# Optimization experiments

Measured on AMD Instinct MI355X. Metric: run time of the kernel, lower is better.

Reference implementation:

```python
import jax, jax.numpy as jnp
import numpy as np

T, B, I, H, O, L = 256, 128, 128, 512, 1, 5


def setup_inputs() -> dict:
    key = jax.random.key(0)
    ks = jax.random.split(key, 12)
    k = 1.0 / np.sqrt(H)
    u = lambda kk, shape: jax.random.uniform(kk, shape, jnp.float32, -k, k)
    inp = {
        "input_seq": jax.random.normal(ks[0], (T, B, I), jnp.float32),
        # layer 0: input size I, 2 directions
        "W_ih0": u(ks[1], (2, 3 * H, I)),
        "W_hh0": u(ks[2], (2, 3 * H, H)),
        "b_ih0": u(ks[3], (2, 3 * H)),
        "b_hh0": u(ks[4], (2, 3 * H)),
        # layers 1..4: input size 2H, 2 directions
        "W_ih": u(ks[5], (L - 1, 2, 3 * H, 2 * H)),
        "W_hh": u(ks[6], (L - 1, 2, 3 * H, H)),
        "b_ih": u(ks[7], (L - 1, 2, 3 * H)),
        "b_hh": u(ks[8], (L - 1, 2, 3 * H)),
        "fc_w": u(ks[9], (O, 2 * H)),
        "fc_b": u(ks[10], (O,)),
    }
    return inp


def _gru_dir(x, Wih, Whh, bih, bhh):
    # x: [T, B, in]; precompute input-side gates for all timesteps
    gx = jnp.einsum('tbi,gi->tbg', x, Wih) + bih  # [T, B, 3H]

    def step(h, g):
        gh = h @ Whh.T + bhh  # [B, 3H]
        xr, xz, xn = jnp.split(g, 3, axis=-1)
        hr, hz, hn = jnp.split(gh, 3, axis=-1)
        r = jax.nn.sigmoid(xr + hr)
        z = jax.nn.sigmoid(xz + hz)
        n = jnp.tanh(xn + r * hn)
        h_new = (1.0 - z) * n + z * h
        return h_new, h_new

    h0 = jnp.zeros((x.shape[1], Whh.shape[1]), x.dtype)
    _, hs = jax.lax.scan(step, h0, gx)
    return hs  # [T, B, H]


def _bigru_layer(x, Wih, Whh, bih, bhh):
    # Wih: [2, 3H, in]; direction 0 = forward, 1 = backward (PyTorch convention)
    fwd = _gru_dir(x, Wih[0], Whh[0], bih[0], bhh[0])
    bwd = _gru_dir(x[::-1], Wih[1], Whh[1], bih[1], bhh[1])[::-1]
    return jnp.concatenate([fwd, bwd], axis=-1)  # [T, B, 2H]


def reference(input_seq, W_ih0, W_hh0, b_ih0, b_hh0, W_ih, W_hh, b_ih, b_hh, fc_w, fc_b):
    # 5-layer bidirectional GRU (eval mode: inter-layer dropout inactive)
    h = _bigru_layer(input_seq, W_ih0, W_hh0, b_ih0, b_hh0)
    for l in range(L - 1):
        h = _bigru_layer(h, W_ih[l], W_hh[l], b_ih[l], b_hh[l])
    out = jnp.einsum('tbh,oh->tbo', h, fc_w) + fc_b
    return jax.nn.sigmoid(out)
```

## Files before the change

kernel.cpp:

```cpp
#include <hip/hip_runtime.h>
#include <hip/hip_bf16.h>

#define T_ 256
#define B_ 128
#define H_ 512
#define G3 1536
#define SCH 32
#define NCH 8
#define RWG 32
#define BGRP 8

typedef __attribute__((ext_vector_type(8))) short short8;
typedef __attribute__((ext_vector_type(4))) short short4v;
typedef __attribute__((ext_vector_type(4))) float f32x4;

static __device__ __forceinline__ float b2f(short s){
    unsigned u = ((unsigned)(unsigned short)s) << 16;
    return __builtin_bit_cast(float, u);
}
static __device__ __forceinline__ short f2b(float f){
    __hip_bfloat16 h = __float2bfloat16(f);
    return __builtin_bit_cast(short, h);
}
static __device__ __forceinline__ void gload16(const void* g, void* l){
    __builtin_amdgcn_global_load_lds(
        (__attribute__((address_space(1))) void*)(void*)g,
        (__attribute__((address_space(3))) void*)l, 16, 0, 0);
}
static __device__ __forceinline__ short8 gload_sc(const short* p){
    short8 v;
    asm volatile("global_load_dwordx4 %0, %1, off sc0 sc1"
                 : "=v"(v) : "v"(p) : "memory");
    return v;
}
static __device__ __forceinline__ void gstore_sc(short* p, short v){
    asm volatile("global_store_short %0, %1, off sc0 sc1"
                 :: "v"(p), "v"(v) : "memory");
}
static __device__ __forceinline__ void wait_vm0(){
    asm volatile("s_waitcnt vmcnt(0)" ::: "memory");
}

__global__ void cvt_f32_to_bf16(const float* __restrict__ src, short* __restrict__ dst, int n){
    int i = (blockIdx.x * blockDim.x + threadIdx.x) * 4;
    int stride = gridDim.x * blockDim.x * 4;
    for (; i + 3 < n; i += stride){
        float4 v = *(const float4*)(src + i);
        short4v o;
        o[0] = f2b(v.x); o[1] = f2b(v.y); o[2] = f2b(v.z); o[3] = f2b(v.w);
        *(short4v*)(dst + i) = o;
    }
}

__global__ __launch_bounds__(256) void gx_gemm(
    const short* __restrict__ A,
    const short* __restrict__ W,
    const float* __restrict__ bias,
    short* __restrict__ gxc,
    int K, int t0f, int t0b_lo)
{
    __shared__ __align__(16) short sA[4096];
    __shared__ __align__(16) short sB[4096];
    const int dir = blockIdx.z;
    const int t0 = dir ? t0b_lo : t0f;
    const int m0 = blockIdx.x * 128;
    const int n0 = blockIdx.y * 128;
    const short* Ae = A + (size_t)(t0 * B_) * K;
    const short* We = W + (size_t)dir * G3 * K;
    short* out = gxc + (size_t)dir * ((size_t)SCH * B_ * G3);

    const int tid = threadIdx.x, wv = tid >> 6, lane = tid & 63;
    const int moff = (wv & 1) * 64, noff = (wv >> 1) * 64;
    const int e0 = wv * 1024 + lane * 8, e1 = e0 + 512;
    const short* a0 = Ae + (size_t)(m0 + (e0 >> 5)) * K + (e0 & 31);
    const short* a1 = Ae + (size_t)(m0 + (e1 >> 5)) * K + (e1 & 31);
    const short* b0 = We + (size_t)(n0 + (e0 >> 5)) * K + (e0 & 31);
    const short* b1 = We + (size_t)(n0 + (e1 >> 5)) * K + (e1 & 31);
    short* sa0 = &sA[wv * 1024];  short* sa1 = &sA[wv * 1024 + 512];
    short* sb0 = &sB[wv * 1024];  short* sb1 = &sB[wv * 1024 + 512];

    f32x4 acc[4][4] = {};
    const int lr = lane & 15, lk = (lane >> 4) * 8;

    for (int kk = 0; kk < K; kk += 32){
        gload16(a0 + kk, sa0); gload16(a1 + kk, sa1);
        gload16(b0 + kk, sb0); gload16(b1 + kk, sb1);
        __syncthreads();
        short8 ar[4], br[4];
        #pragma unroll
        for (int i = 0; i < 4; ++i) ar[i] = *(const short8*)&sA[(moff + i*16 + lr) * 32 + lk];
        #pragma unroll
        for (int i = 0; i < 4; ++i) br[i] = *(const short8*)&sB[(noff + i*16 + lr) * 32 + lk];
        #pragma unroll
        for (int ai = 0; ai < 4; ++ai)
            #pragma unroll
            for (int bi = 0; bi < 4; ++bi)
                acc[ai][bi] = __builtin_amdgcn_mfma_f32_16x16x32_bf16(ar[ai], br[bi], acc[ai][bi], 0, 0, 0);
        __syncthreads();
    }

    #pragma unroll
    for (int ai = 0; ai < 4; ++ai){
        #pragma unroll
        for (int bi = 0; bi < 4; ++bi){
            int col = n0 + noff + bi*16 + lr;
            float bv = bias[dir * G3 + col];
            #pragma unroll
            for (int r = 0; r < 4; ++r){
                int row = m0 + moff + ai*16 + ((lane >> 4) << 2) + r;
                out[(size_t)row * G3 + col] = f2b(acc[ai][bi][r] + bv);
            }
        }
    }
}

__global__ __launch_bounds__(256, 1) void rec_kernel(
    const short* __restrict__ gxc,
    const short* __restrict__ Whh,
    const float* __restrict__ bhh,
    short* __restrict__ xout,
    float* __restrict__ hfm,
    short* __restrict__ hbb,
    int* __restrict__ bar,
    int t0f, int t0b_hi, int first, int base)
{
    __shared__ __align__(16) short lds_h[32 * 520];
    const int tid = threadIdx.x, wv = tid >> 6, lane = tid & 63;
    const int ug = blockIdx.x >> 2, bg = blockIdx.x & 3, dir = blockIdx.y;
    const int u0 = ug * 64 + wv * 16;
    const int m0 = bg * 32;
    const int lr = lane & 15, lk = (lane >> 4) * 8;
    const int crow = (lane >> 4) * 4;

    const short* Wd = Whh + (size_t)dir * G3 * H_;
    short8 wreg[3][16];
    #pragma unroll
    for (int g = 0; g < 3; ++g)
        #pragma unroll
        for (int kk = 0; kk < 16; ++kk)
            wreg[g][kk] = *(const short8*)&Wd[(size_t)(g*H_ + u0 + lr) * H_ + kk*32 + lk];

    float bh[3];
    #pragma unroll
    for (int g = 0; g < 3; ++g) bh[g] = bhh[dir*G3 + g*H_ + u0 + lr];

    float hreg[2][4];
    #pragma unroll
    for (int mt = 0; mt < 2; ++mt)
        #pragma unroll
        for (int r = 0; r < 4; ++r)
            hreg[mt][r] = first ? 0.f
                : hfm[((size_t)dir*B_ + m0 + mt*16 + crow + r)*H_ + u0 + lr];

    int* cnt = bar + (dir*4 + bg) * 32;
    const short* gxd = gxc + (size_t)dir * ((size_t)SCH * B_ * G3);

    const int srow = tid >> 3, scol0 = (tid & 7) * 8;

    float gv[3][2][4];
    {
        const int tl0 = dir ? (SCH - 1) : 0;
        const short* gb = gxd + ((size_t)(tl0 * B_) + m0 + crow) * G3 + u0 + lr;
        #pragma unroll
        for (int g = 0; g < 3; ++g)
            #pragma unroll
            for (int mt = 0; mt < 2; ++mt)
                #pragma unroll
                for (int r = 0; r < 4; ++r)
                    gv[g][mt][r] = b2f(gb[(size_t)(mt*16 + r) * G3 + g * H_]);
    }

    for (int sl = 0; sl < SCH; ++sl){
        const int t  = dir ? (t0b_hi - sl) : (t0f + sl);
        const int rp = sl & 1;

        {
            const short* hsrc = hbb + ((size_t)(rp*2 + dir) * B_ + m0) * H_;
            short8 hv[8];
            #pragma unroll
            for (int c = 0; c < 8; ++c)
                hv[c] = gload_sc(hsrc + (size_t)srow * H_ + scol0 + c*64);
            wait_vm0();
            #pragma unroll
            for (int c = 0; c < 8; ++c)
                *(short8*)&lds_h[srow * 520 + scol0 + c*64] = hv[c];
        }
        __syncthreads();

        f32x4 acc[3][2] = {};
        #pragma unroll
        for (int kk = 0; kk < 16; ++kk){
            short8 a0 = *(const short8*)&lds_h[(lr)      * 520 + kk*32 + lk];
            short8 a1 = *(const short8*)&lds_h[(16 + lr) * 520 + kk*32 + lk];
            #pragma unroll
            for (int g = 0; g < 3; ++g){
                acc[g][0] = __builtin_amdgcn_mfma_f32_16x16x32_bf16(a0, wreg[g][kk], acc[g][0], 0, 0, 0);
                acc[g][1] = __builtin_amdgcn_mfma_f32_16x16x32_bf16(a1, wreg[g][kk], acc[g][1], 0, 0, 0);
            }
        }

        short* hwr = hbb + ((size_t)((rp^1)*2 + dir) * B_) * H_;
        #pragma unroll
        for (int mt = 0; mt < 2; ++mt){
            #pragma unroll
            for (int r = 0; r < 4; ++r){
                float gr = acc[0][mt][r] + bh[0] + gv[0][mt][r];
                float gz = acc[1][mt][r] + bh[1] + gv[1][mt][r];
                float gn = acc[2][mt][r] + bh[2];
                float xn = gv[2][mt][r];
                float rg = 1.f / (1.f + __expf(-gr));
                float zg = 1.f / (1.f + __expf(-gz));
                float e2 = __expf(2.f * (xn + rg * gn));
                float ng = 1.f - 2.f / (e2 + 1.f);
                float hn = (1.f - zg) * ng + zg * hreg[mt][r];
                hreg[mt][r] = hn;
                short h16 = f2b(hn);
                const int row = m0 + mt*16 + crow + r;
                gstore_sc(hwr + (size_t)row * H_ + u0 + lr, h16);
                xout[((size_t)t * B_ + row) * 1024 + dir*H_ + u0 + lr] = h16;
            }
        }

        wait_vm0();
        __syncthreads();
        if (tid == 0)
            __hip_atomic_fetch_add(cnt, 1, __ATOMIC_RELAXED, __HIP_MEMORY_SCOPE_AGENT);

        if (sl + 1 < SCH){
            const int tln = dir ? (SCH - 2 - sl) : (sl + 1);
            const short* gb = gxd + ((size_t)(tln * B_) + m0 + crow) * G3 + u0 + lr;
            #pragma unroll
            for (int g = 0; g < 3; ++g)
                #pragma unroll
                for (int mt = 0; mt < 2; ++mt)
                    #pragma unroll
                    for (int r = 0; r < 4; ++r)
                        gv[g][mt][r] = b2f(gb[(size_t)(mt*16 + r) * G3 + g * H_]);
        }

        if (tid == 0){
            const int tgt = (base + sl + 1) * BGRP;
            while (__hip_atomic_load(cnt, __ATOMIC_RELAXED, __HIP_MEMORY_SCOPE_AGENT) < tgt)
                __builtin_amdgcn_s_sleep(1);
        }
        __syncthreads();
    }

    #pragma unroll
    for (int mt = 0; mt < 2; ++mt)
        #pragma unroll
        for (int r = 0; r < 4; ++r)
            hfm[((size_t)dir*B_ + m0 + mt*16 + crow + r)*H_ + u0 + lr] = hreg[mt][r];
}

__global__ void fc_kernel(const short* __restrict__ h, const float* __restrict__ w,
                          const float* __restrict__ b, float* __restrict__ out){
    int wid = threadIdx.x >> 6, lane = threadIdx.x & 63;
    int tb = blockIdx.x * 4 + wid;
    const short* hp = h + (size_t)tb * 1024 + lane * 16;
    float s = 0.f;
    #pragma unroll
    for (int c = 0; c < 2; ++c){
        short8 v = *(const short8*)(hp + c * 8);
        #pragma unroll
        for (int e = 0; e < 8; ++e) s += b2f(v[e]) * w[lane * 16 + c * 8 + e];
    }
    #pragma unroll
    for (int o = 32; o; o >>= 1) s += __shfl_down(s, o);
    if (lane == 0) out[tb] = 1.f / (1.f + __expf(-(s + b[0])));
}

extern "C" void kernel_launch(void* const* d_in, const int* in_sizes, int n_in,
                              void* d_out, int out_size, void* d_ws, size_t ws_size,
                              hipStream_t stream){
    const float* input_seq = (const float*)d_in[0];
    const float* W_ih0 = (const float*)d_in[1];
    const float* W_hh0 = (const float*)d_in[2];
    const float* b_ih0 = (const float*)d_in[3];
    const float* b_hh0 = (const float*)d_in[4];
    const float* W_ih  = (const float*)d_in[5];
    const float* W_hh  = (const float*)d_in[6];
    const float* b_ih  = (const float*)d_in[7];
    const float* b_hh  = (const float*)d_in[8];
    const float* fc_w  = (const float*)d_in[9];
    const float* fc_b  = (const float*)d_in[10];
    (void)in_sizes; (void)n_in; (void)out_size; (void)ws_size;

    char* ws = (char*)d_ws;
    size_t off = 0;
    auto alloc = [&](size_t bytes) -> char* {
        char* p = ws + off; off += (bytes + 255) & ~(size_t)255; return p;
    };
    short* actA = (short*)alloc((size_t)T_*B_*1024 * 2);
    short* actB = (short*)alloc((size_t)T_*B_*1024 * 2);
    short* gxc  = (short*)alloc((size_t)2*SCH*B_*G3 * 2);
    short* wihl = (short*)alloc((size_t)2*G3*1024 * 2);
    short* whhl = (short*)alloc((size_t)2*G3*H_ * 2);
    float* hfm  = (float*)alloc((size_t)2*B_*H_ * 4);
    short* hbb  = (short*)alloc((size_t)2*2*B_*H_ * 2);
    int*   bar  = (int*)alloc(4096);

    auto cvt = [&](const float* s, short* d, size_t n){
        int blocks = (int)((n/4 + 255) / 256); if (blocks > 4096) blocks = 4096;
        hipLaunchKernelGGL(cvt_f32_to_bf16, dim3(blocks), dim3(256), 0, stream, s, d, (int)n);
    };

    cvt(input_seq, actB, (size_t)T_*B_*128);

    for (int l = 0; l < 5; ++l){
        const int K = l ? 1024 : 128;
        cvt(l ? W_ih + (size_t)(l-1)*2*G3*1024 : W_ih0, wihl, (size_t)2*G3*K);
        cvt(l ? W_hh + (size_t)(l-1)*2*G3*H_   : W_hh0, whhl, (size_t)2*G3*H_);
        const short* IN  = (l & 1) ? actA : actB;
        short*       OUT = (l & 1) ? actB : actA;
        const float* bi = l ? b_ih + (size_t)(l-1)*2*G3 : b_ih0;
        const float* bh = l ? b_hh + (size_t)(l-1)*2*G3 : b_hh0;

        hipMemsetAsync(hbb, 0, (size_t)2*2*B_*H_*2, stream);
        hipMemsetAsync(bar, 0, 4096, stream);

        for (int q = 0; q < NCH; ++q){
            const int t0f    = SCH * q;
            const int t0b_hi = T_ - 1 - SCH * q;
            const int t0b_lo = t0b_hi - SCH + 1;
            hipLaunchKernelGGL(gx_gemm, dim3(SCH*B_/128, G3/128, 2), dim3(256), 0, stream,
                               IN, wihl, bi, gxc, K, t0f, t0b_lo);
            hipLaunchKernelGGL(rec_kernel, dim3(RWG, 2), dim3(256), 0, stream,
                               gxc, whhl, bh, OUT, hfm, hbb, bar, t0f, t0b_hi, q == 0, q*SCH);
        }
    }
    hipLaunchKernelGGL(fc_kernel, dim3((T_*B_)/4), dim3(256), 0, stream,
                       actA, fc_w, fc_b, (float*)d_out);
}
```

Before: 6.799 ms.

## Interleave both GRU directions in one workgroup and stage gate inputs in LDS

Each recurrence workgroup now owns both the forward and backward direction for its unit/batch slice and alternates between them every timestep, halving the grid. The grid-wide barrier wait for one direction can then overlap with the other direction's compute. Input-gate values are prefetched asynchronously into a double-buffered LDS array instead of scattered register loads. In exchange, the recurrent weight registers double, which risks spills at one wave per SIMD, and only half as many CUs carry the serial recurrence.

```diff
diff --git a/kernel.cpp b/kernel.cpp
--- a/kernel.cpp
+++ b/kernel.cpp
@@ -125,132 +125,140 @@
     int t0f, int t0b_hi, int first, int base)
 {
     __shared__ __align__(16) short lds_h[32 * 520];
+    __shared__ __align__(16) short lds_gx[2][2][3 * 2048];
     const int tid = threadIdx.x, wv = tid >> 6, lane = tid & 63;
-    const int ug = blockIdx.x >> 2, bg = blockIdx.x & 3, dir = blockIdx.y;
-    const int u0 = ug * 64 + wv * 16;
+    const int ug = blockIdx.x >> 2, bg = blockIdx.x & 3;
+    const int u0w = ug * 64;
+    const int u0 = u0w + wv * 16;
     const int m0 = bg * 32;
     const int lr = lane & 15, lk = (lane >> 4) * 8;
     const int crow = (lane >> 4) * 4;
-
-    const short* Wd = Whh + (size_t)dir * G3 * H_;
-    short8 wreg[3][16];
-    #pragma unroll
-    for (int g = 0; g < 3; ++g)
-        #pragma unroll
-        for (int kk = 0; kk < 16; ++kk)
-            wreg[g][kk] = *(const short8*)&Wd[(size_t)(g*H_ + u0 + lr) * H_ + kk*32 + lk];
-
-    float bh[3];
-    #pragma unroll
-    for (int g = 0; g < 3; ++g) bh[g] = bhh[dir*G3 + g*H_ + u0 + lr];
-
-    float hreg[2][4];
-    #pragma unroll
-    for (int mt = 0; mt < 2; ++mt)
-        #pragma unroll
-        for (int r = 0; r < 4; ++r)
-            hreg[mt][r] = first ? 0.f
-                : hfm[((size_t)dir*B_ + m0 + mt*16 + crow + r)*H_ + u0 + lr];
-
-    int* cnt = bar + (dir*4 + bg) * 32;
-    const short* gxd = gxc + (size_t)dir * ((size_t)SCH * B_ * G3);
-
     const int srow = tid >> 3, scol0 = (tid & 7) * 8;
-
-    float gv[3][2][4];
-    {
-        const int tl0 = dir ? (SCH - 1) : 0;
-        const short* gb = gxd + ((size_t)(tl0 * B_) + m0 + crow) * G3 + u0 + lr;
+    const int uw = wv * 16 + lr;
+
+    short8 wreg[2][3][16];
+    #pragma unroll
+    for (int d = 0; d < 2; ++d)
         #pragma unroll
         for (int g = 0; g < 3; ++g)
             #pragma unroll
-            for (int mt = 0; mt < 2; ++mt)
+            for (int kk = 0; kk < 16; ++kk)
+                wreg[d][g][kk] = *(const short8*)&Whh[
+                    ((size_t)(d*G3 + g*H_ + u0 + lr)) * H_ + kk*32 + lk];
+
+    float bh[2][3];
+    #pragma unroll
+    for (int d = 0; d < 2; ++d)
+        #pragma unroll
+        for (int g = 0; g < 3; ++g)
+            bh[d][g] = bhh[d*G3 + g*H_ + u0 + lr];
+
+    float hreg[2][2][4];
+    #pragma unroll
+    for (int d = 0; d < 2; ++d)
+        #pragma unroll
+        for (int mt = 0; mt < 2; ++mt)
+            #pragma unroll
+            for (int r = 0; r < 4; ++r)
+                hreg[d][mt][r] = first ? 0.f
+                    : hfm[((size_t)d*B_ + m0 + mt*16 + crow + r)*H_ + u0 + lr];
+
+    #pragma unroll
+    for (int d = 0; d < 2; ++d){
+        const int tl0 = d ? (SCH - 1) : 0;
+        const short* gsrc = gxc + (size_t)d * ((size_t)SCH * B_ * G3)
+                          + ((size_t)(tl0 * B_) + m0 + srow) * G3 + u0w + scol0;
+        #pragma unroll
+        for (int g = 0; g < 3; ++g)
+            gload16(gsrc + g * H_, &lds_gx[d][0][g * 2048 + tid * 8]);
+    }
+
+    for (int sl = 0; sl < SCH; ++sl){
+        const int rp = sl & 1;
+        #pragma unroll
+        for (int d = 0; d < 2; ++d){
+            const int t  = d ? (t0b_hi - sl) : (t0f + sl);
+            int* cnt = bar + (bg*2 + d) * 32;
+
+            if (tid == 0){
+                const int tgt = (base + sl) * BGRP;
+                while (__hip_atomic_load(cnt, __ATOMIC_RELAXED, __HIP_MEMORY_SCOPE_AGENT) < tgt)
+                    __builtin_amdgcn_s_sleep(1);
+            }
+            __syncthreads();
+
+            {
+                const short* hsrc = hbb + ((size_t)(rp*2 + d) * B_ + m0) * H_;
+                short8 hv[8];
                 #pragma unroll
-                for (int r = 0; r < 4; ++r)
-                    gv[g][mt][r] = b2f(gb[(size_t)(mt*16 + r) * G3 + g * H_]);
-    }
-
-    for (int sl = 0; sl < SCH; ++sl){
-        const int t  = dir ? (t0b_hi - sl) : (t0f + sl);
-        const int rp = sl & 1;
-
-        {
-            const short* hsrc = hbb + ((size_t)(rp*2 + dir) * B_ + m0) * H_;
-            short8 hv[8];
-            #pragma unroll
-            for (int c = 0; c < 8; ++c)
-                hv[c] = gload_sc(hsrc + (size_t)srow * H_ + scol0 + c*64);
+                for (int c = 0; c < 8; ++c)
+                    hv[c] = gload_sc(hsrc + (size_t)srow * H_ + scol0 + c*64);
+                if (sl + 1 < SCH){
+                    const int tln = d ? (SCH - 2 - sl) : (sl + 1);
+                    const short* gsrc = gxc + (size_t)d * ((size_t)SCH * B_ * G3)
+                                      + ((size_t)(tln * B_) + m0 + srow) * G3 + u0w + scol0;
+                    #pragma unroll
+                    for (int g = 0; g < 3; ++g)
+                        gload16(gsrc + g * H_, &lds_gx[d][rp ^ 1][g * 2048 + tid * 8]);
+                }
+                wait_vm0();
+                #pragma unroll
+                for (int c = 0; c < 8; ++c)
+                    *(short8*)&lds_h[srow * 520 + scol0 + c*64] = hv[c];
+            }
+            __syncthreads();
+
+            f32x4 acc[3][2] = {};
+            #pragma unroll
+            for (int kk = 0; kk < 16; ++kk){
+                short8 a0 = *(const short8*)&lds_h[(lr)      * 520 + kk*32 + lk];
+                short8 a1 = *(const short8*)&lds_h[(16 + lr) * 520 + kk*32 + lk];
+                #pragma unroll
+                for (int g = 0; g < 3; ++g){
+                    acc[g][0] = __builtin_amdgcn_mfma_f32_16x16x32_bf16(a0, wreg[d][g][kk], acc[g][0], 0, 0, 0);
+                    acc[g][1] = __builtin_amdgcn_mfma_f32_16x16x32_bf16(a1, wreg[d][g][kk], acc[g][1], 0, 0, 0);
+                }
+            }
+
+            short* hwr = hbb + ((size_t)((rp^1)*2 + d) * B_) * H_;
+            #pragma unroll
+            for (int mt = 0; mt < 2; ++mt){
+                #pragma unroll
+                for (int r = 0; r < 4; ++r){
+                    const int lrow = mt*16 + crow + r;
+                    const int row  = m0 + lrow;
+                    float xr = b2f(lds_gx[d][rp][0*2048 + lrow * 64 + uw]);
+                    float xz = b2f(lds_gx[d][rp][1*2048 + lrow * 64 + uw]);
+                    float xn = b2f(lds_gx[d][rp][2*2048 + lrow * 64 + uw]);
+                    float gr = acc[0][mt][r] + bh[d][0] + xr;
+                    float gz = acc[1][mt][r] + bh[d][1] + xz;
+                    float gn = acc[2][mt][r] + bh[d][2];
+                    float rg = 1.f / (1.f + __expf(-gr));
+                    float zg = 1.f / (1.f + __expf(-gz));
+                    float e2 = __expf(2.f * (xn + rg * gn));
+                    float ng = 1.f - 2.f / (e2 + 1.f);
+                    float hn = (1.f - zg) * ng + zg * hreg[d][mt][r];
+                    hreg[d][mt][r] = hn;
+                    short h16 = f2b(hn);
+                    gstore_sc(hwr + (size_t)row * H_ + u0 + lr, h16);
+                    xout[((size_t)t * B_ + row) * 1024 + d*H_ + u0 + lr] = h16;
+                }
+            }
+
             wait_vm0();
-            #pragma unroll
-            for (int c = 0; c < 8; ++c)
-                *(short8*)&lds_h[srow * 520 + scol0 + c*64] = hv[c];
+            __syncthreads();
+            if (tid == 0)
+                __hip_atomic_fetch_add(cnt, 1, __ATOMIC_RELAXED, __HIP_MEMORY_SCOPE_AGENT);
         }
-        __syncthreads();
-
-        f32x4 acc[3][2] = {};
-        #pragma unroll
-        for (int kk = 0; kk < 16; ++kk){
-            short8 a0 = *(const short8*)&lds_h[(lr)      * 520 + kk*32 + lk];
-            short8 a1 = *(const short8*)&lds_h[(16 + lr) * 520 + kk*32 + lk];
-            #pragma unroll
-            for (int g = 0; g < 3; ++g){
-                acc[g][0] = __builtin_amdgcn_mfma_f32_16x16x32_bf16(a0, wreg[g][kk], acc[g][0], 0, 0, 0);
-                acc[g][1] = __builtin_amdgcn_mfma_f32_16x16x32_bf16(a1, wreg[g][kk], acc[g][1], 0, 0, 0);
-            }
-        }
-
-        short* hwr = hbb + ((size_t)((rp^1)*2 + dir) * B_) * H_;
-        #pragma unroll
-        for (int mt = 0; mt < 2; ++mt){
-            #pragma unroll
-            for (int r = 0; r < 4; ++r){
-                float gr = acc[0][mt][r] + bh[0] + gv[0][mt][r];
-                float gz = acc[1][mt][r] + bh[1] + gv[1][mt][r];
-                float gn = acc[2][mt][r] + bh[2];
-                float xn = gv[2][mt][r];
-                float rg = 1.f / (1.f + __expf(-gr));
-                float zg = 1.f / (1.f + __expf(-gz));
-                float e2 = __expf(2.f * (xn + rg * gn));
-                float ng = 1.f - 2.f / (e2 + 1.f);
-                float hn = (1.f - zg) * ng + zg * hreg[mt][r];
-                hreg[mt][r] = hn;
-                short h16 = f2b(hn);
-                const int row = m0 + mt*16 + crow + r;
-                gstore_sc(hwr + (size_t)row * H_ + u0 + lr, h16);
-                xout[((size_t)t * B_ + row) * 1024 + dir*H_ + u0 + lr] = h16;
-            }
-        }
-
-        wait_vm0();
-        __syncthreads();
-        if (tid == 0)
-            __hip_atomic_fetch_add(cnt, 1, __ATOMIC_RELAXED, __HIP_MEMORY_SCOPE_AGENT);
-
-        if (sl + 1 < SCH){
-            const int tln = dir ? (SCH - 2 - sl) : (sl + 1);
-            const short* gb = gxd + ((size_t)(tln * B_) + m0 + crow) * G3 + u0 + lr;
-            #pragma unroll
-            for (int g = 0; g < 3; ++g)
-                #pragma unroll
-                for (int mt = 0; mt < 2; ++mt)
-                    #pragma unroll
-                    for (int r = 0; r < 4; ++r)
-                        gv[g][mt][r] = b2f(gb[(size_t)(mt*16 + r) * G3 + g * H_]);
-        }
-
-        if (tid == 0){
-            const int tgt = (base + sl + 1) * BGRP;
-            while (__hip_atomic_load(cnt, __ATOMIC_RELAXED, __HIP_MEMORY_SCOPE_AGENT) < tgt)
-                __builtin_amdgcn_s_sleep(1);
-        }
-        __syncthreads();
-    }
-
-    #pragma unroll
-    for (int mt = 0; mt < 2; ++mt)
-        #pragma unroll
-        for (int r = 0; r < 4; ++r)
-            hfm[((size_t)dir*B_ + m0 + mt*16 + crow + r)*H_ + u0 + lr] = hreg[mt][r];
+    }
+
+    #pragma unroll
+    for (int d = 0; d < 2; ++d)
+        #pragma unroll
+        for (int mt = 0; mt < 2; ++mt)
+            #pragma unroll
+            for (int r = 0; r < 4; ++r)
+                hfm[((size_t)d*B_ + m0 + mt*16 + crow + r)*H_ + u0 + lr] = hreg[d][mt][r];
 }
 
 __global__ void fc_kernel(const short* __restrict__ h, const float* __restrict__ w,
@@ -325,7 +333,7 @@
             const int t0b_lo = t0b_hi - SCH + 1;
             hipLaunchKernelGGL(gx_gemm, dim3(SCH*B_/128, G3/128, 2), dim3(256), 0, stream,
                                IN, wihl, bi, gxc, K, t0f, t0b_lo);
-            hipLaunchKernelGGL(rec_kernel, dim3(RWG, 2), dim3(256), 0, stream,
+            hipLaunchKernelGGL(rec_kernel, dim3(RWG), dim3(256), 0, stream,
                                gxc, whhl, bh, OUT, hfm, hbb, bar, t0f, t0b_hi, q == 0, q*SCH);
         }
     }
```

After: 13.37 ms. +96.6%, slower.

## Split each GRU step into two half-batch phases with staggered barrier counters

Applied to the files above, without the earlier changes.

The recurrent kernel now processes each timestep as two 16-row half-batch phases instead of one 32-row block. Each half has its own cross-block counter, so the wait for one half's hidden state can overlap with computing the other half. The signal for a finished phase is posted after the next phase's loads, and the gx loads move into the phase itself. The aim is to hide inter-workgroup barrier latency on the serial recurrence, at the cost of twice as many barrier waits and smaller MFMA batches per phase.

```diff
diff --git a/kernel.cpp b/kernel.cpp
--- a/kernel.cpp
+++ b/kernel.cpp
@@ -124,13 +124,14 @@
     int* __restrict__ bar,
     int t0f, int t0b_hi, int first, int base)
 {
-    __shared__ __align__(16) short lds_h[32 * 520];
+    __shared__ __align__(16) short lds_h[2][16 * 520];
     const int tid = threadIdx.x, wv = tid >> 6, lane = tid & 63;
     const int ug = blockIdx.x >> 2, bg = blockIdx.x & 3, dir = blockIdx.y;
     const int u0 = ug * 64 + wv * 16;
     const int m0 = bg * 32;
     const int lr = lane & 15, lk = (lane >> 4) * 8;
     const int crow = (lane >> 4) * 4;
+    const int srow = tid >> 4, scol0 = (tid & 15) * 32;
 
     const short* Wd = Whh + (size_t)dir * G3 * H_;
     short8 wreg[3][16];
@@ -146,111 +147,93 @@
 
     float hreg[2][4];
     #pragma unroll
-    for (int mt = 0; mt < 2; ++mt)
+    for (int hf = 0; hf < 2; ++hf)
         #pragma unroll
         for (int r = 0; r < 4; ++r)
-            hreg[mt][r] = first ? 0.f
-                : hfm[((size_t)dir*B_ + m0 + mt*16 + crow + r)*H_ + u0 + lr];
-
-    int* cnt = bar + (dir*4 + bg) * 32;
+            hreg[hf][r] = first ? 0.f
+                : hfm[((size_t)dir*B_ + m0 + hf*16 + crow + r)*H_ + u0 + lr];
+
+    int* cntA = bar + (dir*4 + bg) * 32;
+    int* cntB = cntA + 16;
     const short* gxd = gxc + (size_t)dir * ((size_t)SCH * B_ * G3);
 
-    const int srow = tid >> 3, scol0 = (tid & 7) * 8;
-
-    float gv[3][2][4];
-    {
-        const int tl0 = dir ? (SCH - 1) : 0;
-        const short* gb = gxd + ((size_t)(tl0 * B_) + m0 + crow) * G3 + u0 + lr;
+    for (int ph = 0; ph < 2 * SCH; ++ph){
+        const int half = ph & 1, sl = ph >> 1;
+        const int rp = sl & 1;
+        int* cnt     = half ? cntB : cntA;
+        int* cntPrev = half ? cntA : cntB;
+
+        if (tid == 0){
+            const int tgt = (base + sl) * BGRP;
+            while (__hip_atomic_load(cnt, __ATOMIC_RELAXED, __HIP_MEMORY_SCOPE_AGENT) < tgt)
+                __builtin_amdgcn_s_sleep(1);
+        }
+        __syncthreads();
+
+        const short* hsrc = hbb + ((size_t)(rp*2 + dir) * B_ + m0 + half*16) * H_;
+        short8 hv[4];
+        #pragma unroll
+        for (int c = 0; c < 4; ++c)
+            hv[c] = gload_sc(hsrc + (size_t)srow * H_ + scol0 + c*8);
+
+        const int tl = dir ? (SCH - 1 - sl) : sl;
+        const short* gb = gxd + ((size_t)(tl * B_) + m0 + half*16 + crow) * G3 + u0 + lr;
+        float gv[3][4];
         #pragma unroll
         for (int g = 0; g < 3; ++g)
             #pragma unroll
-            for (int mt = 0; mt < 2; ++mt)
-                #pragma unroll
-                for (int r = 0; r < 4; ++r)
-                    gv[g][mt][r] = b2f(gb[(size_t)(mt*16 + r) * G3 + g * H_]);
-    }
-
-    for (int sl = 0; sl < SCH; ++sl){
-        const int t  = dir ? (t0b_hi - sl) : (t0f + sl);
-        const int rp = sl & 1;
-
-        {
-            const short* hsrc = hbb + ((size_t)(rp*2 + dir) * B_ + m0) * H_;
-            short8 hv[8];
-            #pragma unroll
-            for (int c = 0; c < 8; ++c)
-                hv[c] = gload_sc(hsrc + (size_t)srow * H_ + scol0 + c*64);
-            wait_vm0();
-            #pragma unroll
-            for (int c = 0; c < 8; ++c)
-                *(short8*)&lds_h[srow * 520 + scol0 + c*64] = hv[c];
-        }
+            for (int r = 0; r < 4; ++r)
+                gv[g][r] = b2f(gb[(size_t)r * G3 + g * H_]);
+
+        wait_vm0();
+        #pragma unroll
+        for (int c = 0; c < 4; ++c)
+            *(short8*)&lds_h[half][srow * 520 + scol0 + c*8] = hv[c];
         __syncthreads();
 
-        f32x4 acc[3][2] = {};
+        if (ph > 0 && tid == 0)
+            __hip_atomic_fetch_add(cntPrev, 1, __ATOMIC_RELAXED, __HIP_MEMORY_SCOPE_AGENT);
+
+        f32x4 acc[3] = {};
         #pragma unroll
         for (int kk = 0; kk < 16; ++kk){
-            short8 a0 = *(const short8*)&lds_h[(lr)      * 520 + kk*32 + lk];
-            short8 a1 = *(const short8*)&lds_h[(16 + lr) * 520 + kk*32 + lk];
-            #pragma unroll
-            for (int g = 0; g < 3; ++g){
-                acc[g][0] = __builtin_amdgcn_mfma_f32_16x16x32_bf16(a0, wreg[g][kk], acc[g][0], 0, 0, 0);
-                acc[g][1] = __builtin_amdgcn_mfma_f32_16x16x32_bf16(a1, wreg[g][kk], acc[g][1], 0, 0, 0);
-            }
-        }
-
-        short* hwr = hbb + ((size_t)((rp^1)*2 + dir) * B_) * H_;
-        #pragma unroll
-        for (int mt = 0; mt < 2; ++mt){
-            #pragma unroll
-            for (int r = 0; r < 4; ++r){
-                float gr = acc[0][mt][r] + bh[0] + gv[0][mt][r];
-                float gz = acc[1][mt][r] + bh[1] + gv[1][mt][r];
-                float gn = acc[2][mt][r] + bh[2];
-                float xn = gv[2][mt][r];
-                float rg = 1.f / (1.f + __expf(-gr));
-                float zg = 1.f / (1.f + __expf(-gz));
-                float e2 = __expf(2.f * (xn + rg * gn));
-                float ng = 1.f - 2.f / (e2 + 1.f);
-                float hn = (1.f - zg) * ng + zg * hreg[mt][r];
-                hreg[mt][r] = hn;
-                short h16 = f2b(hn);
-                const int row = m0 + mt*16 + crow + r;
-                gstore_sc(hwr + (size_t)row * H_ + u0 + lr, h16);
-                xout[((size_t)t * B_ + row) * 1024 + dir*H_ + u0 + lr] = h16;
-            }
-        }
-
-        wait_vm0();
-        __syncthreads();
-        if (tid == 0)
-            __hip_atomic_fetch_add(cnt, 1, __ATOMIC_RELAXED, __HIP_MEMORY_SCOPE_AGENT);
-
-        if (sl + 1 < SCH){
-            const int tln = dir ? (SCH - 2 - sl) : (sl + 1);
-            const short* gb = gxd + ((size_t)(tln * B_) + m0 + crow) * G3 + u0 + lr;
+            short8 a = *(const short8*)&lds_h[half][lr * 520 + kk*32 + lk];
             #pragma unroll
             for (int g = 0; g < 3; ++g)
-                #pragma unroll
-                for (int mt = 0; mt < 2; ++mt)
-                    #pragma unroll
-                    for (int r = 0; r < 4; ++r)
-                        gv[g][mt][r] = b2f(gb[(size_t)(mt*16 + r) * G3 + g * H_]);
-        }
-
-        if (tid == 0){
-            const int tgt = (base + sl + 1) * BGRP;
-            while (__hip_atomic_load(cnt, __ATOMIC_RELAXED, __HIP_MEMORY_SCOPE_AGENT) < tgt)
-                __builtin_amdgcn_s_sleep(1);
-        }
-        __syncthreads();
-    }
-
-    #pragma unroll
-    for (int mt = 0; mt < 2; ++mt)
+                acc[g] = __builtin_amdgcn_mfma_f32_16x16x32_bf16(a, wreg[g][kk], acc[g], 0, 0, 0);
+        }
+
+        const int t = dir ? (t0b_hi - sl) : (t0f + sl);
+        short* hwr = hbb + ((size_t)((rp^1)*2 + dir) * B_) * H_;
+        #pragma unroll
+        for (int r = 0; r < 4; ++r){
+            float gr = acc[0][r] + bh[0] + gv[0][r];
+            float gz = acc[1][r] + bh[1] + gv[1][r];
+            float gn = acc[2][r] + bh[2];
+            float xn = gv[2][r];
+            float rg = 1.f / (1.f + __expf(-gr));
+            float zg = 1.f / (1.f + __expf(-gz));
+            float e2 = __expf(2.f * (xn + rg * gn));
+            float ng = 1.f - 2.f / (e2 + 1.f);
+            float hn = (1.f - zg) * ng + zg * hreg[half][r];
+            hreg[half][r] = hn;
+            short h16 = f2b(hn);
+            const int row = m0 + half*16 + crow + r;
+            gstore_sc(hwr + (size_t)row * H_ + u0 + lr, h16);
+            xout[((size_t)t * B_ + row) * 1024 + dir*H_ + u0 + lr] = h16;
+        }
+    }
+
+    wait_vm0();
+    __syncthreads();
+    if (tid == 0)
+        __hip_atomic_fetch_add(cntB, 1, __ATOMIC_RELAXED, __HIP_MEMORY_SCOPE_AGENT);
+
+    #pragma unroll
+    for (int hf = 0; hf < 2; ++hf)
         #pragma unroll
         for (int r = 0; r < 4; ++r)
-            hfm[((size_t)dir*B_ + m0 + mt*16 + crow + r)*H_ + u0 + lr] = hreg[mt][r];
+            hfm[((size_t)dir*B_ + m0 + hf*16 + crow + r)*H_ + u0 + lr] = hreg[hf][r];
 }
 
 __global__ void fc_kernel(const short* __restrict__ h, const float* __restrict__ w,
```

Result: slower. 9.104 ms (+33.9%).

## Fuse next-chunk input GEMM into recurrence kernel and use per-block step flags

Applied to the files above, without the earlier changes.

The recurrence kernel now also launches extra workgroups that compute the input-gate GEMM for the next time chunk into a double buffer, so that GEMM runs alongside the sequential recurrence instead of between launches. The atomic counter barrier is replaced by per-workgroup step flags, and the previous hidden state is read straight from the layer output instead of a separate ping-pong buffer. Outputs are staged in LDS and written with 16-byte stores. Chunk size is halved to 16 with 16 chunks, which doubles the launch count but allows finer overlap. Risks include contention between the GEMM and recurrence blocks and the requirement that all 64 recurrence blocks be co-resident for the spin-wait.

```diff
diff --git a/kernel.cpp b/kernel.cpp
--- a/kernel.cpp
+++ b/kernel.cpp
@@ -5,14 +5,15 @@
 #define B_ 128
 #define H_ 512
 #define G3 1536
-#define SCH 32
-#define NCH 8
-#define RWG 32
+#define SCH 16
+#define NCH 16
 #define BGRP 8
+#define GXWG 384
 
 typedef __attribute__((ext_vector_type(8))) short short8;
 typedef __attribute__((ext_vector_type(4))) short short4v;
 typedef __attribute__((ext_vector_type(4))) float f32x4;
+typedef __attribute__((ext_vector_type(4))) unsigned int uint4v;
 
 static __device__ __forceinline__ float b2f(short s){
     unsigned u = ((unsigned)(unsigned short)s) << 16;
@@ -26,6 +27,9 @@
     __builtin_amdgcn_global_load_lds(
         (__attribute__((address_space(1))) void*)(void*)g,
         (__attribute__((address_space(3))) void*)l, 16, 0, 0);
+}
+static __device__ __forceinline__ void wait_vm0(){
+    asm volatile("s_waitcnt vmcnt(0)" ::: "memory");
 }
 static __device__ __forceinline__ short8 gload_sc(const short* p){
     short8 v;
@@ -33,12 +37,22 @@
                  : "=v"(v) : "v"(p) : "memory");
     return v;
 }
-static __device__ __forceinline__ void gstore_sc(short* p, short v){
-    asm volatile("global_store_short %0, %1, off sc0 sc1"
+static __device__ __forceinline__ void gstore16_sc(short* p, short8 v){
+    asm volatile("global_store_dwordx4 %0, %1, off sc0 sc1"
                  :: "v"(p), "v"(v) : "memory");
 }
-static __device__ __forceinline__ void wait_vm0(){
-    asm volatile("s_waitcnt vmcnt(0)" ::: "memory");
+static __device__ __forceinline__ void store_flag(unsigned int* p, unsigned int v){
+    asm volatile("global_store_dword %0, %1, off sc0 sc1"
+                 :: "v"(p), "v"(v) : "memory");
+}
+static __device__ __forceinline__ void load_flags8(const unsigned int* p, unsigned int* f){
+    uint4v a, b;
+    asm volatile("global_load_dwordx4 %0, %2, off sc0 sc1\n\t"
+                 "global_load_dwordx4 %1, %3, off sc0 sc1\n\t"
+                 "s_waitcnt vmcnt(0)"
+                 : "=v"(a), "=v"(b) : "v"(p), "v"(p + 4) : "memory");
+    f[0]=a.x; f[1]=a.y; f[2]=a.z; f[3]=a.w;
+    f[4]=b.x; f[5]=b.y; f[6]=b.z; f[7]=b.w;
 }
 
 __global__ void cvt_f32_to_bf16(const float* __restrict__ src, short* __restrict__ dst, int n){
@@ -52,24 +66,14 @@
     }
 }
 
-__global__ __launch_bounds__(256) void gx_gemm(
-    const short* __restrict__ A,
-    const short* __restrict__ W,
-    const float* __restrict__ bias,
-    short* __restrict__ gxc,
-    int K, int t0f, int t0b_lo)
+static __device__ void gx_tile(const short* __restrict__ Ae,
+                               const short* __restrict__ We,
+                               const float* __restrict__ bias_d,
+                               short* __restrict__ out,
+                               int K, int m0, int n0, int tid,
+                               short* sA, short* sB)
 {
-    __shared__ __align__(16) short sA[4096];
-    __shared__ __align__(16) short sB[4096];
-    const int dir = blockIdx.z;
-    const int t0 = dir ? t0b_lo : t0f;
-    const int m0 = blockIdx.x * 128;
-    const int n0 = blockIdx.y * 128;
-    const short* Ae = A + (size_t)(t0 * B_) * K;
-    const short* We = W + (size_t)dir * G3 * K;
-    short* out = gxc + (size_t)dir * ((size_t)SCH * B_ * G3);
-
-    const int tid = threadIdx.x, wv = tid >> 6, lane = tid & 63;
+    const int wv = tid >> 6, lane = tid & 63;
     const int moff = (wv & 1) * 64, noff = (wv >> 1) * 64;
     const int e0 = wv * 1024 + lane * 8, e1 = e0 + 512;
     const short* a0 = Ae + (size_t)(m0 + (e0 >> 5)) * K + (e0 & 31);
@@ -104,7 +108,7 @@
         #pragma unroll
         for (int bi = 0; bi < 4; ++bi){
             int col = n0 + noff + bi*16 + lr;
-            float bv = bias[dir * G3 + col];
+            float bv = bias_d[col];
             #pragma unroll
             for (int r = 0; r < 4; ++r){
                 int row = m0 + moff + ai*16 + ((lane >> 4) << 2) + r;
@@ -114,23 +118,61 @@
     }
 }
 
-__global__ __launch_bounds__(256, 1) void rec_kernel(
-    const short* __restrict__ gxc,
+__global__ __launch_bounds__(256) void gx_gemm(
+    const short* __restrict__ A, const short* __restrict__ W,
+    const float* __restrict__ bias, short* __restrict__ gxc,
+    int K, int t0f, int t0b_lo)
+{
+    __shared__ __align__(16) short sA[4096];
+    __shared__ __align__(16) short sB[4096];
+    const int dir = blockIdx.z;
+    const int t0 = dir ? t0b_lo : t0f;
+    gx_tile(A + (size_t)(t0 * B_) * K, W + (size_t)dir * G3 * K, bias + dir * G3,
+            gxc + (size_t)dir * ((size_t)SCH * B_ * G3),
+            K, blockIdx.x * 128, blockIdx.y * 128, threadIdx.x, sA, sB);
+}
+
+__global__ __launch_bounds__(256, 1) void fused_step(
+    const short* __restrict__ gxc_cur,
+    const short* __restrict__ IN,
+    const short* __restrict__ Wih,
+    const float* __restrict__ bih,
+    short* __restrict__ gxc_nxt,
     const short* __restrict__ Whh,
     const float* __restrict__ bhh,
     short* __restrict__ xout,
     float* __restrict__ hfm,
-    short* __restrict__ hbb,
-    int* __restrict__ bar,
-    int t0f, int t0b_hi, int first, int base)
+    unsigned int* __restrict__ flags,
+    int K, int t0f_n, int t0b_lo_n,
+    int base, int first)
 {
     __shared__ __align__(16) short lds_h[32 * 520];
-    const int tid = threadIdx.x, wv = tid >> 6, lane = tid & 63;
-    const int ug = blockIdx.x >> 2, bg = blockIdx.x & 3, dir = blockIdx.y;
-    const int u0 = ug * 64 + wv * 16;
+    __shared__ __align__(16) short lds_out[32 * 72];
+    __shared__ __align__(16) short sA[4096];
+    __shared__ __align__(16) short sB[4096];
+    const int tid = threadIdx.x;
+    const int bid = blockIdx.x;
+
+    if (bid >= 64){
+        const int idx = bid - 64;
+        const int mi = idx & 15, ni = (idx >> 4) % 12, dr = idx / 192;
+        const int t0 = dr ? t0b_lo_n : t0f_n;
+        gx_tile(IN + (size_t)(t0 * B_) * K, Wih + (size_t)dr * G3 * K, bih + dr * G3,
+                gxc_nxt + (size_t)dr * ((size_t)SCH * B_ * G3),
+                K, mi * 128, ni * 128, tid, sA, sB);
+        return;
+    }
+
+    const int wv = tid >> 6, lane = tid & 63;
+    const int ug = bid >> 3, gid = bid & 7;
+    const int dir = gid >> 2, bg = gid & 3;
+    const int u0w = ug * 64;
+    const int u0 = u0w + wv * 16;
     const int m0 = bg * 32;
     const int lr = lane & 15, lk = (lane >> 4) * 8;
     const int crow = (lane >> 4) * 4;
+    const int srow = tid >> 3, scol = (tid & 7) * 64;
+    const int t0f = base, t0b_hi = T_ - 1 - base;
 
     const short* Wd = Whh + (size_t)dir * G3 * H_;
     short8 wreg[3][16];
@@ -152,10 +194,8 @@
             hreg[mt][r] = first ? 0.f
                 : hfm[((size_t)dir*B_ + m0 + mt*16 + crow + r)*H_ + u0 + lr];
 
-    int* cnt = bar + (dir*4 + bg) * 32;
-    const short* gxd = gxc + (size_t)dir * ((size_t)SCH * B_ * G3);
-
-    const int srow = tid >> 3, scol0 = (tid & 7) * 8;
+    unsigned int* flg = flags + gid * 32;
+    const short* gxd = gxc_cur + (size_t)dir * ((size_t)SCH * B_ * G3);
 
     float gv[3][2][4];
     {
@@ -171,19 +211,38 @@
     }
 
     for (int sl = 0; sl < SCH; ++sl){
+        const int sg = base + sl;
         const int t  = dir ? (t0b_hi - sl) : (t0f + sl);
-        const int rp = sl & 1;
-
-        {
-            const short* hsrc = hbb + ((size_t)(rp*2 + dir) * B_ + m0) * H_;
+
+        if (tid == 0){
+            unsigned int f[8];
+            for (;;){
+                load_flags8(flg, f);
+                bool ok = true;
+                #pragma unroll
+                for (int j = 0; j < 8; ++j) ok &= (f[j] >= (unsigned int)sg);
+                if (ok) break;
+                __builtin_amdgcn_s_sleep(1);
+            }
+        }
+        __syncthreads();
+
+        if (first && sl == 0){
+            short8 z = {};
+            #pragma unroll
+            for (int c = 0; c < 8; ++c)
+                *(short8*)&lds_h[srow * 520 + scol + c*8] = z;
+        } else {
+            const int tprev = dir ? (t + 1) : (t - 1);
+            const short* hsrc = xout + ((size_t)tprev * B_ + m0 + srow) * 1024 + dir*H_;
             short8 hv[8];
             #pragma unroll
             for (int c = 0; c < 8; ++c)
-                hv[c] = gload_sc(hsrc + (size_t)srow * H_ + scol0 + c*64);
+                hv[c] = gload_sc(hsrc + scol + c*8);
             wait_vm0();
             #pragma unroll
             for (int c = 0; c < 8; ++c)
-                *(short8*)&lds_h[srow * 520 + scol0 + c*64] = hv[c];
+                *(short8*)&lds_h[srow * 520 + scol + c*8] = hv[c];
         }
         __syncthreads();
 
@@ -199,7 +258,6 @@
             }
         }
 
-        short* hwr = hbb + ((size_t)((rp^1)*2 + dir) * B_) * H_;
         #pragma unroll
         for (int mt = 0; mt < 2; ++mt){
             #pragma unroll
@@ -214,17 +272,20 @@
                 float ng = 1.f - 2.f / (e2 + 1.f);
                 float hn = (1.f - zg) * ng + zg * hreg[mt][r];
                 hreg[mt][r] = hn;
-                short h16 = f2b(hn);
-                const int row = m0 + mt*16 + crow + r;
-                gstore_sc(hwr + (size_t)row * H_ + u0 + lr, h16);
-                xout[((size_t)t * B_ + row) * 1024 + dir*H_ + u0 + lr] = h16;
+                lds_out[(mt*16 + crow + r) * 72 + wv*16 + lr] = f2b(hn);
             }
         }
-
+        __syncthreads();
+
+        {
+            const int orow = tid >> 3, oc = (tid & 7) * 8;
+            short8 ov = *(const short8*)&lds_out[orow * 72 + oc];
+            gstore16_sc(xout + ((size_t)t * B_ + m0 + orow) * 1024 + dir*H_ + u0w + oc, ov);
+        }
         wait_vm0();
         __syncthreads();
-        if (tid == 0)
-            __hip_atomic_fetch_add(cnt, 1, __ATOMIC_RELAXED, __HIP_MEMORY_SCOPE_AGENT);
+
+        if (tid == 0) store_flag(&flg[ug], (unsigned int)(sg + 1));
 
         if (sl + 1 < SCH){
             const int tln = dir ? (SCH - 2 - sl) : (sl + 1);
@@ -237,13 +298,6 @@
                     for (int r = 0; r < 4; ++r)
                         gv[g][mt][r] = b2f(gb[(size_t)(mt*16 + r) * G3 + g * H_]);
         }
-
-        if (tid == 0){
-            const int tgt = (base + sl + 1) * BGRP;
-            while (__hip_atomic_load(cnt, __ATOMIC_RELAXED, __HIP_MEMORY_SCOPE_AGENT) < tgt)
-                __builtin_amdgcn_s_sleep(1);
-        }
-        __syncthreads();
     }
 
     #pragma unroll
@@ -293,12 +347,12 @@
     };
     short* actA = (short*)alloc((size_t)T_*B_*1024 * 2);
     short* actB = (short*)alloc((size_t)T_*B_*1024 * 2);
-    short* gxc  = (short*)alloc((size_t)2*SCH*B_*G3 * 2);
+    short* gxc0 = (short*)alloc((size_t)2*SCH*B_*G3 * 2);
+    short* gxc1 = (short*)alloc((size_t)2*SCH*B_*G3 * 2);
     short* wihl = (short*)alloc((size_t)2*G3*1024 * 2);
     short* whhl = (short*)alloc((size_t)2*G3*H_ * 2);
     float* hfm  = (float*)alloc((size_t)2*B_*H_ * 4);
-    short* hbb  = (short*)alloc((size_t)2*2*B_*H_ * 2);
-    int*   bar  = (int*)alloc(4096);
+    unsigned int* bar = (unsigned int*)alloc(4096);
 
     auto cvt = [&](const float* s, short* d, size_t n){
         int blocks = (int)((n/4 + 255) / 256); if (blocks > 4096) blocks = 4096;
@@ -306,6 +360,8 @@
     };
 
     cvt(input_seq, actB, (size_t)T_*B_*128);
+
+    short* gxbuf[2] = { gxc0, gxc1 };
 
     for (int l = 0; l < 5; ++l){
         const int K = l ? 1024 : 128;
@@ -316,17 +372,18 @@
         const float* bi = l ? b_ih + (size_t)(l-1)*2*G3 : b_ih0;
         const float* bh = l ? b_hh + (size_t)(l-1)*2*G3 : b_hh0;
 
-        hipMemsetAsync(hbb, 0, (size_t)2*2*B_*H_*2, stream);
         hipMemsetAsync(bar, 0, 4096, stream);
 
+        hipLaunchKernelGGL(gx_gemm, dim3(SCH*B_/128, G3/128, 2), dim3(256), 0, stream,
+                           IN, wihl, bi, gxbuf[0], K, 0, T_ - SCH);
+
         for (int q = 0; q < NCH; ++q){
-            const int t0f    = SCH * q;
-            const int t0b_hi = T_ - 1 - SCH * q;
-            const int t0b_lo = t0b_hi - SCH + 1;
-            hipLaunchKernelGGL(gx_gemm, dim3(SCH*B_/128, G3/128, 2), dim3(256), 0, stream,
-                               IN, wihl, bi, gxc, K, t0f, t0b_lo);
-            hipLaunchKernelGGL(rec_kernel, dim3(RWG, 2), dim3(256), 0, stream,
-                               gxc, whhl, bh, OUT, hfm, hbb, bar, t0f, t0b_hi, q == 0, q*SCH);
+            const int has_gx = (q < NCH - 1);
+            hipLaunchKernelGGL(fused_step, dim3(64 + (has_gx ? GXWG : 0)), dim3(256), 0, stream,
+                               gxbuf[q & 1], IN, wihl, bi, gxbuf[(q + 1) & 1],
+                               whhl, bh, OUT, hfm, bar,
+                               K, (q + 1) * SCH, T_ - (q + 2) * SCH,
+                               q * SCH, q == 0);
         }
     }
     hipLaunchKernelGGL(fc_kernel, dim3((T_*B_)/4), dim3(256), 0, stream,
```

After: 8.112 ms. 19.3% more time.
